# Kernel optimization log

Measured on AMD Instinct MI355X. Metric: run time of the kernel, lower is better.

The kernel has to match this reference:

```python
import jax, jax.numpy as jnp
import numpy as np

B = 1048576
STATE_DIM, HIDDEN, LATENT = 21, 64, 14
LN_EPS = 1e-5
# index map replicating the torch repeat/cat reconstruction of metric attention (13 -> 21)
EXPAND_IDX = np.array([0, 1, 2, 3, 4, 4, 5, 5, 5, 6, 6, 6, 7, 7, 8, 9, 9, 10, 10, 11, 12])


def setup_inputs() -> dict:
    key = jax.random.key(0)
    ks = jax.random.split(key, 20)

    def w(k, shape, fan_in):
        return (jax.random.uniform(k, shape, jnp.float32, -1.0, 1.0) / np.sqrt(fan_in))

    return {
        'state': jax.random.normal(ks[0], (B, STATE_DIM), jnp.float32),
        # encoder
        'W_enc1': w(ks[1], (STATE_DIM, HIDDEN), STATE_DIM),
        'b_enc1': w(ks[2], (HIDDEN,), STATE_DIM),
        'ln_g': jnp.ones((HIDDEN,), jnp.float32),
        'ln_b': jnp.zeros((HIDDEN,), jnp.float32),
        'W_enc2': w(ks[3], (HIDDEN, HIDDEN), HIDDEN),
        'b_enc2': w(ks[4], (HIDDEN,), HIDDEN),
        'W_enc3': w(ks[5], (HIDDEN, LATENT), HIDDEN),
        'b_enc3': w(ks[6], (LATENT,), HIDDEN),
        # decoder
        'W_dec1': w(ks[7], (LATENT, HIDDEN), LATENT),
        'b_dec1': w(ks[8], (HIDDEN,), LATENT),
        'W_dec2': w(ks[9], (HIDDEN, 8), HIDDEN),
        'b_dec2': w(ks[10], (8,), HIDDEN),
        # attention heads
        'W_m': w(ks[11], (STATE_DIM, 13), STATE_DIM),
        'b_m': w(ks[12], (13,), STATE_DIM),
        'W_h': w(ks[13], (STATE_DIM, 6), STATE_DIM),
        'b_h': w(ks[14], (6,), STATE_DIM),
        'W_c': w(ks[15], (STATE_DIM, 4), STATE_DIM),
        'b_c': w(ks[16], (4,), STATE_DIM),
        # learnable head scales (init 1.0 as in torch)
        's_m': jnp.asarray(1.0, jnp.float32),
        's_h': jnp.asarray(1.0, jnp.float32),
        's_c': jnp.asarray(1.0, jnp.float32),
    }


def _normalize(state):
    ns = state
    ns = ns.at[:, 0:2].set(state[:, 0:2] / 3.0)
    ns = ns.at[:, 17].set(state[:, 17] / 2.0)
    ns = ns.at[:, 18].set(state[:, 18] / 4.0)
    ns = ns.at[:, 19].set(jnp.clip(state[:, 19], 0.0, 2.0) / 2.0)
    return ns


def _layernorm(x, g, b):
    mu = jnp.mean(x, axis=-1, keepdims=True)
    var = jnp.mean(jnp.square(x - mu), axis=-1, keepdims=True)
    return (x - mu) / jnp.sqrt(var + LN_EPS) * g + b


def reference(state, W_enc1, b_enc1, ln_g, ln_b, W_enc2, b_enc2, W_enc3, b_enc3,
              W_dec1, b_dec1, W_dec2, b_dec2, W_m, b_m, W_h, b_h, W_c, b_c,
              s_m, s_h, s_c):
    ns = _normalize(state)  # [B, 21]

    metric = jax.nn.softmax(ns @ W_m + b_m, axis=-1) * (jax.nn.sigmoid(s_m) * 2.0)  # [B,13]
    hyp = jax.nn.softmax(ns @ W_h + b_h, axis=-1) * (jax.nn.sigmoid(s_h) * 2.0)      # [B,6]
    curr = jax.nn.softmax(ns @ W_c + b_c, axis=-1) * (jax.nn.sigmoid(s_c) * 2.0)     # [B,4]

    attended = ns * metric[:, EXPAND_IDX]  # [B,21]

    h = jnp.tanh(_layernorm(attended @ W_enc1 + b_enc1, ln_g, ln_b))
    h = jax.nn.relu(h @ W_enc2 + b_enc2)
    latent = h @ W_enc3 + b_enc3  # [B,14]

    d = jax.nn.relu(latent @ W_dec1 + b_dec1)
    corrections = jnp.tanh(d @ W_dec2 + b_dec2)  # [B,8]

    return corrections, latent, metric, hyp, curr
```

## Files before the change

kernel.cpp:

```cpp
#include <hip/hip_runtime.h>

static constexpr int SD = 21, HD = 64, LT = 14;
static constexpr int NFRAG = 36;

typedef _Float16       f16x4  __attribute__((ext_vector_type(4)));
typedef float          f32x4  __attribute__((ext_vector_type(4)));
typedef unsigned       u32x2v __attribute__((ext_vector_type(2)));
typedef unsigned short u16x4v __attribute__((ext_vector_type(4)));
typedef __fp16         pk2    __attribute__((ext_vector_type(2)));

__device__ __forceinline__ float frcp(float x){ return __builtin_amdgcn_rcpf(x); }
__device__ __forceinline__ float frsq(float x){ return __builtin_amdgcn_rsqf(x); }

__device__ __forceinline__ unsigned packrtz(float a, float b){
    pk2 h = __builtin_amdgcn_cvt_pkrtz(a, b);
    union { pk2 h; unsigned u; } u; u.h = h; return u.u;
}
__device__ __forceinline__ unsigned short f16bits(float v){
    _Float16 h = (_Float16)v;
    union { _Float16 h; unsigned short s; } u; u.h = h; return u.s;
}
__device__ __forceinline__ float ftanh(float x){
    x = fminf(15.0f, fmaxf(-15.0f, x));
    float e = __expf(2.0f * x);
    return (e - 1.0f) * frcp(e + 1.0f);
}
template<int NN>
__device__ __forceinline__ void softmax_scale(float (&v)[NN], float gate){
    float mx = v[0];
#pragma unroll
    for (int j = 1; j < NN; ++j) mx = fmaxf(mx, v[j]);
    float s = 0.0f;
#pragma unroll
    for (int j = 0; j < NN; ++j){ v[j] = __expf(v[j] - mx); s += v[j]; }
    float r = frcp(s) * gate;
#pragma unroll
    for (int j = 0; j < NN; ++j) v[j] *= r;
}

union Frag2 { u32x2v u2; unsigned u[2]; f16x4 f; };
union FragH { u16x4v uh; f16x4 f; };

__device__ __forceinline__ f32x4 mfma16(f16x4 a, f16x4 b, f32x4 c){
    return __builtin_amdgcn_mfma_f32_16x16x16f16(a, b, c, 0, 0, 0);
}

__global__ void pack_bfrags(const float* __restrict__ W1, const float* __restrict__ W2,
                            const float* __restrict__ W3, const float* __restrict__ Wd1,
                            const float* __restrict__ Wd2, unsigned* __restrict__ ws)
{
    int t = blockIdx.x * blockDim.x + threadIdx.x;
    if (t >= NFRAG * 64) return;
    int fid = t >> 6, lane = t & 63;
    int g = lane >> 4, c = lane & 15;
    const float* W; int ks16, ct, K, Ncol, ld;
    if (fid < 8)       { W = W1;  ks16 = fid >> 2;    ct = fid & 3;  K = 21; Ncol = 64; ld = 64; }
    else if (fid < 24) { int e = fid - 8;
                         W = W2;  ks16 = e >> 2;      ct = e & 3;    K = 64; Ncol = 64; ld = 64; }
    else if (fid < 28) { W = W3;  ks16 = fid - 24;    ct = 0;        K = 64; Ncol = 14; ld = 14; }
    else if (fid < 32) { W = Wd1; ks16 = 0;           ct = fid - 28; K = 14; Ncol = 64; ld = 64; }
    else               { W = Wd2; ks16 = fid - 32;    ct = 0;        K = 64; Ncol = 8;  ld = 8;  }
    int col = ct*16 + c;
#pragma unroll
    for (int j = 0; j < 2; ++j) {
        int k0 = ks16*16 + g*4 + 2*j;
        float a = (k0     < K && col < Ncol) ? W[k0*ld + col]     : 0.0f;
        float b = (k0 + 1 < K && col < Ncol) ? W[(k0+1)*ld + col] : 0.0f;
        ws[fid*128 + lane*2 + j] = packrtz(a, b);
    }
}

__global__ __launch_bounds__(256) void statenet_mfma4(
    const float* __restrict__ state,
    const unsigned* __restrict__ pw,
    const float* __restrict__ b1,
    const float* __restrict__ lng, const float* __restrict__ lnb,
    const float* __restrict__ b2,  const float* __restrict__ b3,
    const float* __restrict__ bd1, const float* __restrict__ bd2,
    const float* __restrict__ Wm,  const float* __restrict__ bm,
    const float* __restrict__ Wh,  const float* __restrict__ bh,
    const float* __restrict__ Wc,  const float* __restrict__ bc,
    const float* __restrict__ psm, const float* __restrict__ psh,
    const float* __restrict__ psc,
    float* __restrict__ out, int N)
{
    __shared__ __align__(16) unsigned s_buf[4*1152];

    const int tid = threadIdx.x;
    const int w  = tid >> 6, l = tid & 63;
    const int cl = l & 15,  g = l >> 4;
    const long long rowbase = (long long)blockIdx.x * 128 + w * 32;

    unsigned*       at = s_buf + w * 1152;
    unsigned short* hb = reinterpret_cast<unsigned short*>(s_buf) + w * 2304;

    if (l < 32) {
        const long long row = rowbase + l;
        float ns[SD];
        {
            const float* p = state + row * SD;
#pragma unroll
        for (int k = 0; k < SD; ++k) ns[k] = p[k];
        }
        ns[0]  *= (1.0f / 3.0f);
        ns[1]  *= (1.0f / 3.0f);
        ns[17] *= 0.5f;
        ns[18] *= 0.25f;
        ns[19]  = fminf(fmaxf(ns[19], 0.0f), 2.0f) * 0.5f;

        float m[13], hv[6], cv[4];
#pragma unroll
        for (int j = 0; j < 13; ++j) m[j]  = bm[j];
#pragma unroll
        for (int j = 0; j < 6;  ++j) hv[j] = bh[j];
#pragma unroll
        for (int j = 0; j < 4;  ++j) cv[j] = bc[j];
#pragma unroll
        for (int k = 0; k < SD; ++k) {
            float x = ns[k];
#pragma unroll
            for (int j = 0; j < 13; ++j) m[j]  = fmaf(x, Wm[k * 13 + j], m[j]);
#pragma unroll
            for (int j = 0; j < 6;  ++j) hv[j] = fmaf(x, Wh[k * 6 + j], hv[j]);
#pragma unroll
            for (int j = 0; j < 4;  ++j) cv[j] = fmaf(x, Wc[k * 4 + j], cv[j]);
        }
        const float gm = 2.0f * frcp(1.0f + __expf(-psm[0]));
        const float gh = 2.0f * frcp(1.0f + __expf(-psh[0]));
        const float gc = 2.0f * frcp(1.0f + __expf(-psc[0]));
        softmax_scale<13>(m,  gm);
        softmax_scale<6 >(hv, gh);
        softmax_scale<4 >(cv, gc);

        {
            float* pm = out + (long long)22 * N + row * 13;
#pragma unroll
            for (int j = 0; j < 13; ++j) pm[j] = m[j];
            float* ph = out + (long long)35 * N + row * 6;
#pragma unroll
            for (int j = 0; j < 3; ++j)
                reinterpret_cast<float2*>(ph)[j] = make_float2(hv[2*j], hv[2*j+1]);
            float* pc = out + (long long)41 * N + row * 4;
            reinterpret_cast<float4*>(pc)[0] = make_float4(cv[0], cv[1], cv[2], cv[3]);
        }

        constexpr int EIDX[SD] = {0,1,2,3,4,4,5,5,5,6,6,6,7,7,8,9,9,10,10,11,12};
        float atv[SD];
#pragma unroll
        for (int k = 0; k < SD; ++k) atv[k] = ns[k] * m[EIDX[k]];
        const int base = l * 36;
#pragma unroll
        for (int kk = 0; kk < 10; ++kk) at[base + kk] = packrtz(atv[2*kk], atv[2*kk+1]);
        at[base + 10] = packrtz(atv[20], 0.0f);
#pragma unroll
        for (int kk = 11; kk < 16; ++kk) at[base + kk] = 0u;
    }
    __syncthreads();

    float b1c[4], b2c[4], bd1c[4], lgc[4], lbc[4];
#pragma unroll
    for (int t2 = 0; t2 < 4; ++t2) {
        int c2 = cl + 16*t2;
        b1c[t2] = b1[c2];  b2c[t2] = b2[c2];  bd1c[t2] = bd1[c2];
        lgc[t2] = lng[c2]; lbc[t2] = lnb[c2];
    }
    const float b3c  = (cl < 14) ? b3[cl]  : 0.0f;
    const float bd2c = (cl < 8)  ? bd2[cl] : 0.0f;

    const u32x2v* BF2 = reinterpret_cast<const u32x2v*>(pw);
    const f32x4 vzero = {0.0f, 0.0f, 0.0f, 0.0f};

    Frag2 aA[2][2];
#pragma unroll
    for (int m2 = 0; m2 < 2; ++m2)
#pragma unroll
        for (int ks = 0; ks < 2; ++ks)
            aA[m2][ks].u2 = *reinterpret_cast<const u32x2v*>(&at[(m2*16 + cl)*36 + ks*8 + 2*g]);
    __syncthreads();

    f32x4 acc[2][4];
#pragma unroll
    for (int m2 = 0; m2 < 2; ++m2)
#pragma unroll
        for (int ct = 0; ct < 4; ++ct) acc[m2][ct] = vzero;
#pragma unroll
    for (int ct = 0; ct < 4; ++ct)
#pragma unroll
        for (int ks = 0; ks < 2; ++ks) {
            Frag2 bf; bf.u2 = BF2[(ks*4 + ct)*64 + l];
#pragma unroll
            for (int m2 = 0; m2 < 2; ++m2)
                acc[m2][ct] = mfma16(aA[m2][ks].f, bf.f, acc[m2][ct]);
        }
#pragma unroll
    for (int m2 = 0; m2 < 2; ++m2) {
        float s[4], ss[4];
#pragma unroll
        for (int q = 0; q < 4; ++q) {
            float v0 = acc[m2][0][q] + b1c[0], v1 = acc[m2][1][q] + b1c[1];
            float v2 = acc[m2][2][q] + b1c[2], v3 = acc[m2][3][q] + b1c[3];
            acc[m2][0][q] = v0; acc[m2][1][q] = v1; acc[m2][2][q] = v2; acc[m2][3][q] = v3;
            s[q]  = v0 + v1 + v2 + v3;
            ss[q] = v0*v0 + v1*v1 + v2*v2 + v3*v3;
        }
#pragma unroll
        for (int q = 0; q < 4; ++q) {
#pragma unroll
            for (int d = 1; d < 16; d <<= 1) {
                s[q]  += __shfl_xor(s[q],  d, 16);
                ss[q] += __shfl_xor(ss[q], d, 16);
            }
        }
#pragma unroll
        for (int q = 0; q < 4; ++q) {
            float mu   = s[q] * (1.0f/64.0f);
            float var  = ss[q] * (1.0f/64.0f) - mu*mu;
            float istd = frsq(var + 1e-5f);
            int r = m2*16 + g*4 + q;
#pragma unroll
            for (int t2 = 0; t2 < 4; ++t2) {
                float v = ftanh(fmaf((acc[m2][t2][q] - mu) * istd, lgc[t2], lbc[t2]));
                hb[r*72 + cl + 16*t2] = f16bits(v);
            }
        }
    }
    __syncthreads();

    FragH ah[2][4];
#pragma unroll
    for (int m2 = 0; m2 < 2; ++m2)
#pragma unroll
        for (int ks = 0; ks < 4; ++ks)
            ah[m2][ks].uh = *reinterpret_cast<const u16x4v*>(&hb[(m2*16 + cl)*72 + ks*16 + 4*g]);
    f32x4 a2[2][4];
#pragma unroll
    for (int m2 = 0; m2 < 2; ++m2)
#pragma unroll
        for (int ct = 0; ct < 4; ++ct) a2[m2][ct] = vzero;
#pragma unroll
    for (int ct = 0; ct < 4; ++ct)
#pragma unroll
        for (int ks = 0; ks < 4; ++ks) {
            Frag2 bf; bf.u2 = BF2[(8 + ks*4 + ct)*64 + l];
#pragma unroll
            for (int m2 = 0; m2 < 2; ++m2)
                a2[m2][ct] = mfma16(ah[m2][ks].f, bf.f, a2[m2][ct]);
        }
    __syncthreads();
#pragma unroll
    for (int m2 = 0; m2 < 2; ++m2)
#pragma unroll
        for (int q = 0; q < 4; ++q) {
            int r = m2*16 + g*4 + q;
#pragma unroll
            for (int t2 = 0; t2 < 4; ++t2)
                hb[r*72 + cl + 16*t2] = f16bits(fmaxf(a2[m2][t2][q] + b2c[t2], 0.0f));
        }
    __syncthreads();

#pragma unroll
    for (int m2 = 0; m2 < 2; ++m2)
#pragma unroll
        for (int ks = 0; ks < 4; ++ks)
            ah[m2][ks].uh = *reinterpret_cast<const u16x4v*>(&hb[(m2*16 + cl)*72 + ks*16 + 4*g]);
    __syncthreads();
#pragma unroll
    for (int m2 = 0; m2 < 2; ++m2) {
        f32x4 a3 = vzero;
#pragma unroll
        for (int ks = 0; ks < 4; ++ks) {
            Frag2 bf; bf.u2 = BF2[(24 + ks)*64 + l];
            a3 = mfma16(ah[m2][ks].f, bf.f, a3);
        }
#pragma unroll
        for (int q = 0; q < 4; ++q) {
            float lv = a3[q] + b3c;
            int r = m2*16 + g*4 + q;
            if (cl < 14)
                out[(long long)8 * N + (rowbase + r) * 14 + cl] = lv;
            float pv = __shfl_xor(lv, 1);
            if ((cl & 1) == 0)
                at[r*36 + (cl >> 1)] = packrtz(lv, pv);
        }
    }
    __syncthreads();

    Frag2 aD[2];
#pragma unroll
    for (int m2 = 0; m2 < 2; ++m2)
        aD[m2].u2 = *reinterpret_cast<const u32x2v*>(&at[(m2*16 + cl)*36 + 2*g]);
    __syncthreads();
    f32x4 ad[2][4];
#pragma unroll
    for (int m2 = 0; m2 < 2; ++m2)
#pragma unroll
        for (int ct = 0; ct < 4; ++ct) ad[m2][ct] = vzero;
#pragma unroll
    for (int ct = 0; ct < 4; ++ct) {
        Frag2 bf; bf.u2 = BF2[(28 + ct)*64 + l];
#pragma unroll
        for (int m2 = 0; m2 < 2; ++m2)
            ad[m2][ct] = mfma16(aD[m2].f, bf.f, ad[m2][ct]);
    }
#pragma unroll
    for (int m2 = 0; m2 < 2; ++m2)
#pragma unroll
        for (int q = 0; q < 4; ++q) {
            int r = m2*16 + g*4 + q;
#pragma unroll
            for (int t2 = 0; t2 < 4; ++t2)
                hb[r*72 + cl + 16*t2] = f16bits(fmaxf(ad[m2][t2][q] + bd1c[t2], 0.0f));
        }
    __syncthreads();

#pragma unroll
    for (int m2 = 0; m2 < 2; ++m2)
#pragma unroll
        for (int ks = 0; ks < 4; ++ks)
            ah[m2][ks].uh = *reinterpret_cast<const u16x4v*>(&hb[(m2*16 + cl)*72 + ks*16 + 4*g]);
#pragma unroll
    for (int m2 = 0; m2 < 2; ++m2) {
        f32x4 a5 = vzero;
#pragma unroll
        for (int ks = 0; ks < 4; ++ks) {
            Frag2 bf; bf.u2 = BF2[(32 + ks)*64 + l];
            a5 = mfma16(ah[m2][ks].f, bf.f, a5);
        }
#pragma unroll
        for (int q = 0; q < 4; ++q) {
            if (cl < 8)
                out[(rowbase + m2*16 + g*4 + q) * 8 + cl] = ftanh(a5[q] + bd2c);
        }
    }
}

extern "C" void kernel_launch(void* const* d_in, const int* in_sizes, int n_in,
                              void* d_out, int out_size, void* d_ws, size_t ws_size,
                              hipStream_t stream)
{
    const float* state = (const float*)d_in[0];
    const float* W1   = (const float*)d_in[1];
    const float* b1   = (const float*)d_in[2];
    const float* lng  = (const float*)d_in[3];
    const float* lnb  = (const float*)d_in[4];
    const float* W2   = (const float*)d_in[5];
    const float* b2   = (const float*)d_in[6];
    const float* W3   = (const float*)d_in[7];
    const float* b3   = (const float*)d_in[8];
    const float* Wd1  = (const float*)d_in[9];
    const float* bd1  = (const float*)d_in[10];
    const float* Wd2  = (const float*)d_in[11];
    const float* bd2  = (const float*)d_in[12];
    const float* Wm   = (const float*)d_in[13];
    const float* bm   = (const float*)d_in[14];
    const float* Wh   = (const float*)d_in[15];
    const float* bh   = (const float*)d_in[16];
    const float* Wc   = (const float*)d_in[17];
    const float* bc   = (const float*)d_in[18];
    const float* psm  = (const float*)d_in[19];
    const float* psh  = (const float*)d_in[20];
    const float* psc  = (const float*)d_in[21];

    unsigned* pw = (unsigned*)d_ws;

    hipLaunchKernelGGL(pack_bfrags, dim3((NFRAG*64 + 255)/256), dim3(256), 0, stream,
                       W1, W2, W3, Wd1, Wd2, pw);

    const int N = in_sizes[0] / SD;
    hipLaunchKernelGGL(statenet_mfma4, dim3(N / 128), dim3(256), 0, stream,
                       state, pw, b1, lng, lnb, b2, b3, bd1, bd2,
                       Wm, bm, Wh, bh, Wc, bc, psm, psh, psc,
                       (float*)d_out, N);
}
```

Baseline: 127.5 us.

## Process 64 rows per wave so all lanes run the attention prologue

Each wave now handles 64 rows instead of 32, so all 64 lanes run the scalar normalize/attention prologue instead of half of them idling. MFMA stages process four 16-row tiles in two halves, reusing each B fragment across more rows. The grid halves and shared memory doubles to about 36 KB per block. This may lower occupancy and raise register pressure from the larger fragment arrays.

```diff
diff --git a/kernel.cpp b/kernel.cpp
--- a/kernel.cpp
+++ b/kernel.cpp
@@ -70,7 +70,7 @@
     }
 }
 
-__global__ __launch_bounds__(256) void statenet_mfma4(
+__global__ __launch_bounds__(256) void statenet_mfma5(
     const float* __restrict__ state,
     const unsigned* __restrict__ pw,
     const float* __restrict__ b1,
@@ -84,23 +84,23 @@
     const float* __restrict__ psc,
     float* __restrict__ out, int N)
 {
-    __shared__ __align__(16) unsigned s_buf[4*1152];
+    __shared__ __align__(16) unsigned s_buf[4*2304];
 
     const int tid = threadIdx.x;
     const int w  = tid >> 6, l = tid & 63;
     const int cl = l & 15,  g = l >> 4;
-    const long long rowbase = (long long)blockIdx.x * 128 + w * 32;
-
-    unsigned*       at = s_buf + w * 1152;
-    unsigned short* hb = reinterpret_cast<unsigned short*>(s_buf) + w * 2304;
-
-    if (l < 32) {
+    const long long rowbase = (long long)blockIdx.x * 256 + w * 64;
+
+    unsigned*       at = s_buf + w * 2304;
+    unsigned short* hb = reinterpret_cast<unsigned short*>(s_buf) + w * 4608;
+
+    {
         const long long row = rowbase + l;
         float ns[SD];
         {
             const float* p = state + row * SD;
 #pragma unroll
-        for (int k = 0; k < SD; ++k) ns[k] = p[k];
+            for (int k = 0; k < SD; ++k) ns[k] = p[k];
         }
         ns[0]  *= (1.0f / 3.0f);
         ns[1]  *= (1.0f / 3.0f);
@@ -170,112 +170,118 @@
     const u32x2v* BF2 = reinterpret_cast<const u32x2v*>(pw);
     const f32x4 vzero = {0.0f, 0.0f, 0.0f, 0.0f};
 
-    Frag2 aA[2][2];
-#pragma unroll
-    for (int m2 = 0; m2 < 2; ++m2)
+    Frag2 aA[4][2];
+#pragma unroll
+    for (int M = 0; M < 4; ++M)
 #pragma unroll
         for (int ks = 0; ks < 2; ++ks)
-            aA[m2][ks].u2 = *reinterpret_cast<const u32x2v*>(&at[(m2*16 + cl)*36 + ks*8 + 2*g]);
-    __syncthreads();
-
-    f32x4 acc[2][4];
-#pragma unroll
-    for (int m2 = 0; m2 < 2; ++m2)
-#pragma unroll
-        for (int ct = 0; ct < 4; ++ct) acc[m2][ct] = vzero;
-#pragma unroll
-    for (int ct = 0; ct < 4; ++ct)
-#pragma unroll
-        for (int ks = 0; ks < 2; ++ks) {
-            Frag2 bf; bf.u2 = BF2[(ks*4 + ct)*64 + l];
-#pragma unroll
-            for (int m2 = 0; m2 < 2; ++m2)
-                acc[m2][ct] = mfma16(aA[m2][ks].f, bf.f, acc[m2][ct]);
-        }
-#pragma unroll
-    for (int m2 = 0; m2 < 2; ++m2) {
-        float s[4], ss[4];
-#pragma unroll
-        for (int q = 0; q < 4; ++q) {
-            float v0 = acc[m2][0][q] + b1c[0], v1 = acc[m2][1][q] + b1c[1];
-            float v2 = acc[m2][2][q] + b1c[2], v3 = acc[m2][3][q] + b1c[3];
-            acc[m2][0][q] = v0; acc[m2][1][q] = v1; acc[m2][2][q] = v2; acc[m2][3][q] = v3;
-            s[q]  = v0 + v1 + v2 + v3;
-            ss[q] = v0*v0 + v1*v1 + v2*v2 + v3*v3;
-        }
-#pragma unroll
-        for (int q = 0; q < 4; ++q) {
-#pragma unroll
-            for (int d = 1; d < 16; d <<= 1) {
-                s[q]  += __shfl_xor(s[q],  d, 16);
-                ss[q] += __shfl_xor(ss[q], d, 16);
-            }
-        }
-#pragma unroll
-        for (int q = 0; q < 4; ++q) {
-            float mu   = s[q] * (1.0f/64.0f);
-            float var  = ss[q] * (1.0f/64.0f) - mu*mu;
-            float istd = frsq(var + 1e-5f);
-            int r = m2*16 + g*4 + q;
-#pragma unroll
-            for (int t2 = 0; t2 < 4; ++t2) {
-                float v = ftanh(fmaf((acc[m2][t2][q] - mu) * istd, lgc[t2], lbc[t2]));
-                hb[r*72 + cl + 16*t2] = f16bits(v);
-            }
-        }
-    }
-    __syncthreads();
-
-    FragH ah[2][4];
-#pragma unroll
-    for (int m2 = 0; m2 < 2; ++m2)
+            aA[M][ks].u2 = *reinterpret_cast<const u32x2v*>(&at[(M*16 + cl)*36 + ks*8 + 2*g]);
+    __syncthreads();
+
+#pragma unroll
+    for (int mh = 0; mh < 2; ++mh) {
+        f32x4 acc[2][4];
+#pragma unroll
+        for (int m2 = 0; m2 < 2; ++m2)
+#pragma unroll
+            for (int ct = 0; ct < 4; ++ct) acc[m2][ct] = vzero;
+#pragma unroll
+        for (int ct = 0; ct < 4; ++ct)
+#pragma unroll
+            for (int ks = 0; ks < 2; ++ks) {
+                Frag2 bf; bf.u2 = BF2[(ks*4 + ct)*64 + l];
+#pragma unroll
+                for (int m2 = 0; m2 < 2; ++m2)
+                    acc[m2][ct] = mfma16(aA[mh*2 + m2][ks].f, bf.f, acc[m2][ct]);
+            }
+#pragma unroll
+        for (int m2 = 0; m2 < 2; ++m2) {
+            float s[4], ss[4];
+#pragma unroll
+            for (int q = 0; q < 4; ++q) {
+                float v0 = acc[m2][0][q] + b1c[0], v1 = acc[m2][1][q] + b1c[1];
+                float v2 = acc[m2][2][q] + b1c[2], v3 = acc[m2][3][q] + b1c[3];
+                acc[m2][0][q] = v0; acc[m2][1][q] = v1; acc[m2][2][q] = v2; acc[m2][3][q] = v3;
+                s[q]  = v0 + v1 + v2 + v3;
+                ss[q] = v0*v0 + v1*v1 + v2*v2 + v3*v3;
+            }
+#pragma unroll
+            for (int q = 0; q < 4; ++q) {
+#pragma unroll
+                for (int d = 1; d < 16; d <<= 1) {
+                    s[q]  += __shfl_xor(s[q],  d, 16);
+                    ss[q] += __shfl_xor(ss[q], d, 16);
+                }
+            }
+#pragma unroll
+            for (int q = 0; q < 4; ++q) {
+                float mu   = s[q] * (1.0f/64.0f);
+                float var  = ss[q] * (1.0f/64.0f) - mu*mu;
+                float istd = frsq(var + 1e-5f);
+                int r = (mh*2 + m2)*16 + g*4 + q;
+#pragma unroll
+                for (int t2 = 0; t2 < 4; ++t2) {
+                    float v = ftanh(fmaf((acc[m2][t2][q] - mu) * istd, lgc[t2], lbc[t2]));
+                    hb[r*72 + cl + 16*t2] = f16bits(v);
+                }
+            }
+        }
+    }
+    __syncthreads();
+
+    FragH ah[4][4];
+#pragma unroll
+    for (int M = 0; M < 4; ++M)
 #pragma unroll
         for (int ks = 0; ks < 4; ++ks)
-            ah[m2][ks].uh = *reinterpret_cast<const u16x4v*>(&hb[(m2*16 + cl)*72 + ks*16 + 4*g]);
-    f32x4 a2[2][4];
-#pragma unroll
-    for (int m2 = 0; m2 < 2; ++m2)
-#pragma unroll
-        for (int ct = 0; ct < 4; ++ct) a2[m2][ct] = vzero;
-#pragma unroll
-    for (int ct = 0; ct < 4; ++ct)
-#pragma unroll
-        for (int ks = 0; ks < 4; ++ks) {
-            Frag2 bf; bf.u2 = BF2[(8 + ks*4 + ct)*64 + l];
-#pragma unroll
-            for (int m2 = 0; m2 < 2; ++m2)
-                a2[m2][ct] = mfma16(ah[m2][ks].f, bf.f, a2[m2][ct]);
-        }
-    __syncthreads();
-#pragma unroll
-    for (int m2 = 0; m2 < 2; ++m2)
-#pragma unroll
-        for (int q = 0; q < 4; ++q) {
-            int r = m2*16 + g*4 + q;
-#pragma unroll
-            for (int t2 = 0; t2 < 4; ++t2)
-                hb[r*72 + cl + 16*t2] = f16bits(fmaxf(a2[m2][t2][q] + b2c[t2], 0.0f));
-        }
-    __syncthreads();
-
-#pragma unroll
-    for (int m2 = 0; m2 < 2; ++m2)
+            ah[M][ks].uh = *reinterpret_cast<const u16x4v*>(&hb[(M*16 + cl)*72 + ks*16 + 4*g]);
+    __syncthreads();
+#pragma unroll
+    for (int mh = 0; mh < 2; ++mh) {
+        f32x4 a2[2][4];
+#pragma unroll
+        for (int m2 = 0; m2 < 2; ++m2)
+#pragma unroll
+            for (int ct = 0; ct < 4; ++ct) a2[m2][ct] = vzero;
+#pragma unroll
+        for (int ct = 0; ct < 4; ++ct)
+#pragma unroll
+            for (int ks = 0; ks < 4; ++ks) {
+                Frag2 bf; bf.u2 = BF2[(8 + ks*4 + ct)*64 + l];
+#pragma unroll
+                for (int m2 = 0; m2 < 2; ++m2)
+                    a2[m2][ct] = mfma16(ah[mh*2 + m2][ks].f, bf.f, a2[m2][ct]);
+            }
+#pragma unroll
+        for (int m2 = 0; m2 < 2; ++m2)
+#pragma unroll
+            for (int q = 0; q < 4; ++q) {
+                int r = (mh*2 + m2)*16 + g*4 + q;
+#pragma unroll
+                for (int t2 = 0; t2 < 4; ++t2)
+                    hb[r*72 + cl + 16*t2] = f16bits(fmaxf(a2[m2][t2][q] + b2c[t2], 0.0f));
+            }
+    }
+    __syncthreads();
+
+#pragma unroll
+    for (int M = 0; M < 4; ++M)
 #pragma unroll
         for (int ks = 0; ks < 4; ++ks)
-            ah[m2][ks].uh = *reinterpret_cast<const u16x4v*>(&hb[(m2*16 + cl)*72 + ks*16 + 4*g]);
-    __syncthreads();
-#pragma unroll
-    for (int m2 = 0; m2 < 2; ++m2) {
+            ah[M][ks].uh = *reinterpret_cast<const u16x4v*>(&hb[(M*16 + cl)*72 + ks*16 + 4*g]);
+    __syncthreads();
+#pragma unroll
+    for (int M = 0; M < 4; ++M) {
         f32x4 a3 = vzero;
 #pragma unroll
         for (int ks = 0; ks < 4; ++ks) {
             Frag2 bf; bf.u2 = BF2[(24 + ks)*64 + l];
-            a3 = mfma16(ah[m2][ks].f, bf.f, a3);
+            a3 = mfma16(ah[M][ks].f, bf.f, a3);
         }
 #pragma unroll
         for (int q = 0; q < 4; ++q) {
             float lv = a3[q] + b3c;
-            int r = m2*16 + g*4 + q;
+            int r = M*16 + g*4 + q;
             if (cl < 14)
                 out[(long long)8 * N + (rowbase + r) * 14 + cl] = lv;
             float pv = __shfl_xor(lv, 1);
@@ -285,51 +291,54 @@
     }
     __syncthreads();
 
-    Frag2 aD[2];
-#pragma unroll
-    for (int m2 = 0; m2 < 2; ++m2)
-        aD[m2].u2 = *reinterpret_cast<const u32x2v*>(&at[(m2*16 + cl)*36 + 2*g]);
-    __syncthreads();
-    f32x4 ad[2][4];
-#pragma unroll
-    for (int m2 = 0; m2 < 2; ++m2)
-#pragma unroll
-        for (int ct = 0; ct < 4; ++ct) ad[m2][ct] = vzero;
-#pragma unroll
-    for (int ct = 0; ct < 4; ++ct) {
-        Frag2 bf; bf.u2 = BF2[(28 + ct)*64 + l];
-#pragma unroll
-        for (int m2 = 0; m2 < 2; ++m2)
-            ad[m2][ct] = mfma16(aD[m2].f, bf.f, ad[m2][ct]);
-    }
-#pragma unroll
-    for (int m2 = 0; m2 < 2; ++m2)
-#pragma unroll
-        for (int q = 0; q < 4; ++q) {
-            int r = m2*16 + g*4 + q;
-#pragma unroll
-            for (int t2 = 0; t2 < 4; ++t2)
-                hb[r*72 + cl + 16*t2] = f16bits(fmaxf(ad[m2][t2][q] + bd1c[t2], 0.0f));
-        }
-    __syncthreads();
-
-#pragma unroll
-    for (int m2 = 0; m2 < 2; ++m2)
+    Frag2 aD[4];
+#pragma unroll
+    for (int M = 0; M < 4; ++M)
+        aD[M].u2 = *reinterpret_cast<const u32x2v*>(&at[(M*16 + cl)*36 + 2*g]);
+    __syncthreads();
+#pragma unroll
+    for (int mh = 0; mh < 2; ++mh) {
+        f32x4 ad[2][4];
+#pragma unroll
+        for (int m2 = 0; m2 < 2; ++m2)
+#pragma unroll
+            for (int ct = 0; ct < 4; ++ct) ad[m2][ct] = vzero;
+#pragma unroll
+        for (int ct = 0; ct < 4; ++ct) {
+            Frag2 bf; bf.u2 = BF2[(28 + ct)*64 + l];
+#pragma unroll
+            for (int m2 = 0; m2 < 2; ++m2)
+                ad[m2][ct] = mfma16(aD[mh*2 + m2].f, bf.f, ad[m2][ct]);
+        }
+#pragma unroll
+        for (int m2 = 0; m2 < 2; ++m2)
+#pragma unroll
+            for (int q = 0; q < 4; ++q) {
+                int r = (mh*2 + m2)*16 + g*4 + q;
+#pragma unroll
+                for (int t2 = 0; t2 < 4; ++t2)
+                    hb[r*72 + cl + 16*t2] = f16bits(fmaxf(ad[m2][t2][q] + bd1c[t2], 0.0f));
+            }
+    }
+    __syncthreads();
+
+#pragma unroll
+    for (int M = 0; M < 4; ++M)
 #pragma unroll
         for (int ks = 0; ks < 4; ++ks)
-            ah[m2][ks].uh = *reinterpret_cast<const u16x4v*>(&hb[(m2*16 + cl)*72 + ks*16 + 4*g]);
-#pragma unroll
-    for (int m2 = 0; m2 < 2; ++m2) {
+            ah[M][ks].uh = *reinterpret_cast<const u16x4v*>(&hb[(M*16 + cl)*72 + ks*16 + 4*g]);
+#pragma unroll
+    for (int M = 0; M < 4; ++M) {
         f32x4 a5 = vzero;
 #pragma unroll
         for (int ks = 0; ks < 4; ++ks) {
             Frag2 bf; bf.u2 = BF2[(32 + ks)*64 + l];
-            a5 = mfma16(ah[m2][ks].f, bf.f, a5);
+            a5 = mfma16(ah[M][ks].f, bf.f, a5);
         }
 #pragma unroll
         for (int q = 0; q < 4; ++q) {
             if (cl < 8)
-                out[(rowbase + m2*16 + g*4 + q) * 8 + cl] = ftanh(a5[q] + bd2c);
+                out[(rowbase + M*16 + g*4 + q) * 8 + cl] = ftanh(a5[q] + bd2c);
         }
     }
 }
@@ -367,7 +376,7 @@
                        W1, W2, W3, Wd1, Wd2, pw);
 
     const int N = in_sizes[0] / SD;
-    hipLaunchKernelGGL(statenet_mfma4, dim3(N / 128), dim3(256), 0, stream,
+    hipLaunchKernelGGL(statenet_mfma5, dim3(N / 256), dim3(256), 0, stream,
                        state, pw, b1, lng, lnb, b2, b3, bd1, bd2,
                        Wm, bm, Wh, bh, Wc, bc, psm, psh, psc,
                        (float*)d_out, N);
```

New measurement: 137.2 us. 7.6% more time.

## Compute attention-head logits with fp16 MFMA instead of scalar FMAs

Applied to the files above, without the earlier changes.

The three attention-head projections (21→13, 6, 4) move from per-thread scalar FMA loops, which ran on only half the lanes, onto MFMA 16x16x16 fp16 tiles. Their weights are prepacked as extra B fragments. Normalized state is staged in LDS as fp16, the logits are written to a new LDS buffer, and a lane per row then reads them back for the softmax. This removes about 480 serial FMAs per row plus the repeated weight loads, at the cost of two extra barriers, more LDS, and fp16 rounding of the head inputs.

```diff
diff --git a/kernel.cpp b/kernel.cpp
--- a/kernel.cpp
+++ b/kernel.cpp
@@ -1,7 +1,7 @@
 #include <hip/hip_runtime.h>
 
 static constexpr int SD = 21, HD = 64, LT = 14;
-static constexpr int NFRAG = 36;
+static constexpr int NFRAG = 40;
 
 typedef _Float16       f16x4  __attribute__((ext_vector_type(4)));
 typedef float          f32x4  __attribute__((ext_vector_type(4)));
@@ -45,14 +45,38 @@
     return __builtin_amdgcn_mfma_f32_16x16x16f16(a, b, c, 0, 0, 0);
 }
 
+__device__ __forceinline__ float headsW(const float* Wm, const float* Wh,
+                                        const float* Wc, int k, int j){
+    if (j < 13) return Wm[k*13 + j];
+    if (j < 19) return Wh[k*6 + (j - 13)];
+    if (j < 23) return Wc[k*4 + (j - 19)];
+    return 0.0f;
+}
+
 __global__ void pack_bfrags(const float* __restrict__ W1, const float* __restrict__ W2,
                             const float* __restrict__ W3, const float* __restrict__ Wd1,
-                            const float* __restrict__ Wd2, unsigned* __restrict__ ws)
+                            const float* __restrict__ Wd2,
+                            const float* __restrict__ Wm, const float* __restrict__ Wh,
+                            const float* __restrict__ Wc, unsigned* __restrict__ ws)
 {
     int t = blockIdx.x * blockDim.x + threadIdx.x;
     if (t >= NFRAG * 64) return;
     int fid = t >> 6, lane = t & 63;
     int g = lane >> 4, c = lane & 15;
+
+    if (fid >= 36) {
+        int e = fid - 36, ks16 = e >> 1, ct = e & 1;
+        int col = ct*16 + c;
+#pragma unroll
+        for (int j = 0; j < 2; ++j) {
+            int k0 = ks16*16 + g*4 + 2*j;
+            float a = (k0     < SD && col < 23) ? headsW(Wm, Wh, Wc, k0,   col) : 0.0f;
+            float b = (k0 + 1 < SD && col < 23) ? headsW(Wm, Wh, Wc, k0+1, col) : 0.0f;
+            ws[fid*128 + lane*2 + j] = packrtz(a, b);
+        }
+        return;
+    }
+
     const float* W; int ks16, ct, K, Ncol, ld;
     if (fid < 8)       { W = W1;  ks16 = fid >> 2;    ct = fid & 3;  K = 21; Ncol = 64; ld = 64; }
     else if (fid < 24) { int e = fid - 8;
@@ -70,37 +94,41 @@
     }
 }
 
-__global__ __launch_bounds__(256) void statenet_mfma4(
+__global__ __launch_bounds__(256) void statenet_mfma6(
     const float* __restrict__ state,
     const unsigned* __restrict__ pw,
     const float* __restrict__ b1,
     const float* __restrict__ lng, const float* __restrict__ lnb,
     const float* __restrict__ b2,  const float* __restrict__ b3,
     const float* __restrict__ bd1, const float* __restrict__ bd2,
-    const float* __restrict__ Wm,  const float* __restrict__ bm,
-    const float* __restrict__ Wh,  const float* __restrict__ bh,
-    const float* __restrict__ Wc,  const float* __restrict__ bc,
+    const float* __restrict__ bm,  const float* __restrict__ bh,
+    const float* __restrict__ bc,
     const float* __restrict__ psm, const float* __restrict__ psh,
     const float* __restrict__ psc,
     float* __restrict__ out, int N)
 {
     __shared__ __align__(16) unsigned s_buf[4*1152];
+    __shared__ __align__(16) float    s_lg[4*832];
 
     const int tid = threadIdx.x;
     const int w  = tid >> 6, l = tid & 63;
     const int cl = l & 15,  g = l >> 4;
     const long long rowbase = (long long)blockIdx.x * 128 + w * 32;
 
-    unsigned*       at = s_buf + w * 1152;
-    unsigned short* hb = reinterpret_cast<unsigned short*>(s_buf) + w * 2304;
-
+    unsigned*       at  = s_buf + w * 1152;
+    unsigned short* hb  = reinterpret_cast<unsigned short*>(s_buf) + w * 2304;
+    float*          slg = s_lg + w * 832;
+
+    const float bc0 = (cl < 13) ? bm[cl] : bh[cl - 13];
+    const float bc1 = (cl < 3) ? bh[cl + 3] : ((cl < 7) ? bc[cl - 3] : 0.0f);
+
+    float ns[SD];
     if (l < 32) {
         const long long row = rowbase + l;
-        float ns[SD];
         {
             const float* p = state + row * SD;
 #pragma unroll
-        for (int k = 0; k < SD; ++k) ns[k] = p[k];
+            for (int k = 0; k < SD; ++k) ns[k] = p[k];
         }
         ns[0]  *= (1.0f / 3.0f);
         ns[1]  *= (1.0f / 3.0f);
@@ -108,23 +136,65 @@
         ns[18] *= 0.25f;
         ns[19]  = fminf(fmaxf(ns[19], 0.0f), 2.0f) * 0.5f;
 
+        const int base = l * 36;
+#pragma unroll
+        for (int kk = 0; kk < 10; ++kk) at[base + kk] = packrtz(ns[2*kk], ns[2*kk+1]);
+        at[base + 10] = packrtz(ns[20], 0.0f);
+#pragma unroll
+        for (int kk = 11; kk < 16; ++kk) at[base + kk] = 0u;
+    }
+    __syncthreads();
+
+    const u32x2v* BF2 = reinterpret_cast<const u32x2v*>(pw);
+    const f32x4 vzero = {0.0f, 0.0f, 0.0f, 0.0f};
+    {
+        Frag2 aN[2][2];
+#pragma unroll
+        for (int m2 = 0; m2 < 2; ++m2)
+#pragma unroll
+            for (int ks = 0; ks < 2; ++ks)
+                aN[m2][ks].u2 = *reinterpret_cast<const u32x2v*>(&at[(m2*16 + cl)*36 + ks*8 + 2*g]);
+        f32x4 hl[2][2];
+#pragma unroll
+        for (int m2 = 0; m2 < 2; ++m2)
+#pragma unroll
+            for (int ct = 0; ct < 2; ++ct) hl[m2][ct] = vzero;
+#pragma unroll
+        for (int ct = 0; ct < 2; ++ct)
+#pragma unroll
+            for (int ks = 0; ks < 2; ++ks) {
+                Frag2 bf; bf.u2 = BF2[(36 + ks*2 + ct)*64 + l];
+#pragma unroll
+                for (int m2 = 0; m2 < 2; ++m2)
+                    hl[m2][ct] = mfma16(aN[m2][ks].f, bf.f, hl[m2][ct]);
+            }
+#pragma unroll
+        for (int m2 = 0; m2 < 2; ++m2)
+#pragma unroll
+            for (int q = 0; q < 4; ++q) {
+                int r = m2*16 + g*4 + q;
+                slg[r*26 + cl] = hl[m2][0][q] + bc0;
+                if (cl < 8) slg[r*26 + 16 + cl] = hl[m2][1][q] + bc1;
+            }
+    }
+    __syncthreads();
+
+    if (l < 32) {
+        const long long row = rowbase + l;
+        float lg[24];
+#pragma unroll
+        for (int i = 0; i < 12; ++i) {
+            float2 v = *reinterpret_cast<const float2*>(&slg[l*26 + 2*i]);
+            lg[2*i] = v.x; lg[2*i+1] = v.y;
+        }
         float m[13], hv[6], cv[4];
 #pragma unroll
-        for (int j = 0; j < 13; ++j) m[j]  = bm[j];
-#pragma unroll
-        for (int j = 0; j < 6;  ++j) hv[j] = bh[j];
-#pragma unroll
-        for (int j = 0; j < 4;  ++j) cv[j] = bc[j];
-#pragma unroll
-        for (int k = 0; k < SD; ++k) {
-            float x = ns[k];
-#pragma unroll
-            for (int j = 0; j < 13; ++j) m[j]  = fmaf(x, Wm[k * 13 + j], m[j]);
-#pragma unroll
-            for (int j = 0; j < 6;  ++j) hv[j] = fmaf(x, Wh[k * 6 + j], hv[j]);
-#pragma unroll
-            for (int j = 0; j < 4;  ++j) cv[j] = fmaf(x, Wc[k * 4 + j], cv[j]);
-        }
+        for (int j = 0; j < 13; ++j) m[j]  = lg[j];
+#pragma unroll
+        for (int j = 0; j < 6;  ++j) hv[j] = lg[13 + j];
+#pragma unroll
+        for (int j = 0; j < 4;  ++j) cv[j] = lg[19 + j];
+
         const float gm = 2.0f * frcp(1.0f + __expf(-psm[0]));
         const float gh = 2.0f * frcp(1.0f + __expf(-psh[0]));
         const float gc = 2.0f * frcp(1.0f + __expf(-psc[0]));
@@ -152,8 +222,6 @@
 #pragma unroll
         for (int kk = 0; kk < 10; ++kk) at[base + kk] = packrtz(atv[2*kk], atv[2*kk+1]);
         at[base + 10] = packrtz(atv[20], 0.0f);
-#pragma unroll
-        for (int kk = 11; kk < 16; ++kk) at[base + kk] = 0u;
     }
     __syncthreads();
 
@@ -166,9 +234,6 @@
     }
     const float b3c  = (cl < 14) ? b3[cl]  : 0.0f;
     const float bd2c = (cl < 8)  ? bd2[cl] : 0.0f;
-
-    const u32x2v* BF2 = reinterpret_cast<const u32x2v*>(pw);
-    const f32x4 vzero = {0.0f, 0.0f, 0.0f, 0.0f};
 
     Frag2 aA[2][2];
 #pragma unroll
@@ -364,11 +429,11 @@
     unsigned* pw = (unsigned*)d_ws;
 
     hipLaunchKernelGGL(pack_bfrags, dim3((NFRAG*64 + 255)/256), dim3(256), 0, stream,
-                       W1, W2, W3, Wd1, Wd2, pw);
+                       W1, W2, W3, Wd1, Wd2, Wm, Wh, Wc, pw);
 
     const int N = in_sizes[0] / SD;
-    hipLaunchKernelGGL(statenet_mfma4, dim3(N / 128), dim3(256), 0, stream,
+    hipLaunchKernelGGL(statenet_mfma6, dim3(N / 128), dim3(256), 0, stream,
                        state, pw, b1, lng, lnb, b2, b3, bd1, bd2,
-                       Wm, bm, Wh, bh, Wc, bc, psm, psh, psc,
+                       bm, bh, bc, psm, psh, psc,
                        (float*)d_out, N);
 }
```

Result: no change. 128.6 us (+0.8%).
